# Kernel optimization log

Measured on AMD Instinct MI355X. Metric: run time of the kernel, lower is better.

## Reference

```python
import jax, jax.numpy as jnp
import numpy as np

HEADS = 8
DIM_HEAD = 64
WINDOW = 8  # local_window_size


def _sn_weight(W, u, sigma):
    """SNLinear reparameterized weight: one power-iteration step (detached)
    then sigma_W = v^T W u (grad flows through W only), weight = W/sigma_W * sigma."""
    v = W @ u
    v = v / jnp.linalg.norm(v)
    u2 = W.T @ v
    u2 = u2 / jnp.linalg.norm(u2)
    v = jax.lax.stop_gradient(v)
    u2 = jax.lax.stop_gradient(u2)
    sigma_w = jnp.einsum('c,cd,d->', v, W, u2)
    return W / sigma_w * sigma


def setup_inputs() -> dict:
    key = jax.random.key(0)
    ks = jax.random.split(key, 6)
    B, S, D = 2, 2048, 512
    inner = HEADS * DIM_HEAD  # 512
    x = jax.random.normal(ks[0], (B, S, D), dtype=jnp.float32)
    W_qkv = 0.02 * jax.random.normal(ks[1], (3 * inner, D), dtype=jnp.float32)
    u_qkv = jax.random.normal(ks[2], (D,), dtype=jnp.float32)
    u_qkv = u_qkv / jnp.linalg.norm(u_qkv)
    W_out = 0.02 * jax.random.normal(ks[3], (D, inner), dtype=jnp.float32)
    b_out = jnp.zeros((D,), dtype=jnp.float32)
    u_out = jax.random.normal(ks[4], (inner,), dtype=jnp.float32)
    u_out = u_out / jnp.linalg.norm(u_out)
    sigma_qkv = jnp.ones((1,), dtype=jnp.float32)
    sigma_out = jnp.ones((1,), dtype=jnp.float32)
    temperature = jnp.asarray(np.log(DIM_HEAD ** -0.5), dtype=jnp.float32)
    return {
        'x': x, 'W_qkv': W_qkv, 'u_qkv': u_qkv, 'sigma_qkv': sigma_qkv,
        'W_out': W_out, 'b_out': b_out, 'u_out': u_out, 'sigma_out': sigma_out,
        'temperature': temperature,
    }


def reference(x, W_qkv, u_qkv, sigma_qkv, W_out, b_out, u_out, sigma_out, temperature):
    B, S, D = x.shape
    # qkv projection (spectral-normed, no bias)
    Wq = _sn_weight(W_qkv, u_qkv, sigma_qkv[0])
    qkv = x @ Wq.T                                   # [B,S,3*inner]
    q, k, v = jnp.split(qkv, 3, axis=-1)
    to_heads = lambda t: t.reshape(B, S, HEADS, DIM_HEAD).transpose(0, 2, 1, 3)
    q, k, v = to_heads(q), to_heads(k), to_heads(v)   # [B,H,S,Dh]
    dots = jnp.einsum('bhid,bhjd->bhij', q, k) * jnp.exp(temperature)
    # local causal band mask (True inside band); original masked_fill fills True
    i = jnp.arange(S)
    band = (i[:, None] >= i[None, :]) & ((i[:, None] - i[None, :]) <= (WINDOW - 1))
    neg = -jnp.finfo(dots.dtype).max
    dots = jnp.where(band[None, None, :, :], neg, dots)
    attn = jax.nn.softmax(dots, axis=-1)
    out = jnp.einsum('bhij,bhjd->bhid', attn, v)      # [B,H,S,Dh]
    out = out.transpose(0, 2, 1, 3).reshape(B, S, HEADS * DIM_HEAD)
    Wo = _sn_weight(W_out, u_out, sigma_out[0])
    return out @ Wo.T + b_out
```

## Files before the change

kernel.cpp:

```cpp
#include <hip/hip_runtime.h>
#include <hip/hip_bf16.h>
#include <math.h>

#define HEADS 8
#define DH 64
#define SEQ 2048
#define BATCH 2
#define DMODEL 512
#define INNER 512
#define WIN 8

typedef unsigned short ushort_t;
typedef __attribute__((ext_vector_type(8))) __bf16 bf16x8;
typedef __attribute__((ext_vector_type(8))) unsigned short u16x8;
typedef __attribute__((ext_vector_type(4))) float f32x4;

__device__ inline float bf2f(ushort_t u) {
    unsigned v = ((unsigned)u) << 16; float f; __builtin_memcpy(&f, &v, 4); return f;
}
__device__ inline ushort_t f2bf(float f) {
    __hip_bfloat16 h = __float2bfloat16(f); ushort_t u; __builtin_memcpy(&u, &h, 2); return u;
}
__device__ inline float fast_exp2(float x) { return __builtin_amdgcn_exp2f(x); }
__device__ inline int swz_idx(int row, int col) { return ((row << 6) | col) ^ ((row & 7) << 3); }

__device__ inline bf16x8 ld_frag(const ushort_t* lds, int row, int col) {
    u16x8 v = *(const u16x8*)&lds[swz_idx(row, col)];
    return __builtin_bit_cast(bf16x8, v);
}
__device__ inline f32x4 mfma16(bf16x8 a, bf16x8 b, f32x4 c) {
    return __builtin_amdgcn_mfma_f32_16x16x32_bf16(a, b, c, 0, 0, 0);
}
__device__ inline void gload16(const void* g, void* l) {
    __builtin_amdgcn_global_load_lds(
        (const __attribute__((address_space(1))) unsigned int*)g,
        (__attribute__((address_space(3))) unsigned int*)l, 16, 0, 0);
}

__global__ __launch_bounds__(256) void fused_cast_sn1(const float* __restrict__ x,
                                                      const float* __restrict__ Wq,
                                                      const float* __restrict__ Wo,
                                                      const float* __restrict__ uq,
                                                      const float* __restrict__ uo,
                                                      ushort_t* __restrict__ xb,
                                                      ushort_t* __restrict__ wqb,
                                                      ushort_t* __restrict__ wob,
                                                      float* __restrict__ zbuf,
                                                      float* __restrict__ v1,
                                                      float* __restrict__ v2) {
    const int b = blockIdx.x;
    if (b < 1536) {
        const int gid = b * 256 + threadIdx.x;
        const float* src; ushort_t* dst; int g;
        if (gid < 262144)      { src = x;  dst = xb;  g = gid; }
        else if (gid < 360448) { src = Wq; dst = wqb; g = gid - 262144; }
        else                   { src = Wo; dst = wob; g = gid - 360448; }
        float4 a = *(const float4*)&src[(size_t)g * 8];
        float4 c = *(const float4*)&src[(size_t)g * 8 + 4];
        u16x8 o;
        o[0] = f2bf(a.x); o[1] = f2bf(a.y); o[2] = f2bf(a.z); o[3] = f2bf(a.w);
        o[4] = f2bf(c.x); o[5] = f2bf(c.y); o[6] = f2bf(c.z); o[7] = f2bf(c.w);
        *(u16x8*)&dst[(size_t)g * 8] = o;
        if (gid < 1032) zbuf[gid] = 0.f;
    } else {
        const int lane = threadIdx.x & 63, w = threadIdx.x >> 6;
        const int r = (b - 1536) * 4 + w;
        const float* W; const float* u; float* vout; int rr;
        if (r < 1536) { W = Wq; u = uq; vout = v1; rr = r; }
        else          { W = Wo; u = uo; vout = v2; rr = r - 1536; }
        float4 w0 = *(const float4*)&W[(size_t)rr * 512 + lane * 8];
        float4 w1 = *(const float4*)&W[(size_t)rr * 512 + lane * 8 + 4];
        float4 u0 = *(const float4*)&u[lane * 8];
        float4 u1 = *(const float4*)&u[lane * 8 + 4];
        float dot = w0.x * u0.x + w0.y * u0.y + w0.z * u0.z + w0.w * u0.w +
                    w1.x * u1.x + w1.y * u1.y + w1.z * u1.z + w1.w * u1.w;
#pragma unroll
        for (int off = 1; off < 64; off <<= 1) dot += __shfl_xor(dot, off, 64);
        if (lane == 0) vout[rr] = dot;
    }
}

__global__ __launch_bounds__(256) void gemm_qkv_sn(const ushort_t* __restrict__ A,
                                                   const ushort_t* __restrict__ B,
                                                   ushort_t* __restrict__ qkv,
                                                   const float* __restrict__ Wq,
                                                   const float* __restrict__ Wo,
                                                   const float* __restrict__ v1,
                                                   const float* __restrict__ v2,
                                                   float* __restrict__ z1,
                                                   float* __restrict__ z2,
                                                   float* __restrict__ counter,
                                                   const float* __restrict__ sq,
                                                   const float* __restrict__ so,
                                                   float* __restrict__ scales) {
    constexpr int K = DMODEL;
    __shared__ ushort_t As[8 * 128 * 8];
    __shared__ ushort_t Bs[8 * 64 * 8];
    __shared__ float red[256];
    __shared__ int is_last;
    const int t = threadIdx.x;

    if (blockIdx.x >= 768) {
        const int b = blockIdx.x - 768;
        {
            const float* W; const float* v; float* z; int r0;
            if (b < 96) { W = Wq; v = v1; z = z1; r0 = b * 16; }
            else        { W = Wo; v = v2; z = z2; r0 = (b - 96) * 16; }
            float a0 = 0.f, a1 = 0.f;
            for (int i = 0; i < 16; ++i) {
                float vv = v[r0 + i];
                a0 += W[(size_t)(r0 + i) * 512 + t] * vv;
                a1 += W[(size_t)(r0 + i) * 512 + 256 + t] * vv;
            }
            atomicAdd(&z[t], a0);
            atomicAdd(&z[t + 256], a1);
        }
        __threadfence();
        __syncthreads();
        if (t == 0) is_last = (atomicAdd(counter, 1.0f) == 127.0f);
        __syncthreads();
        if (!is_last) return;
        __threadfence();
        for (int which = 0; which < 2; ++which) {
            const float* v = which ? v2 : v1;
            const float* z = which ? z2 : z1;
            const int R = which ? 512 : 1536;
            float n1 = 0.f;
            for (int i = t; i < R; i += 256) { float q = v[i]; n1 += q * q; }
            red[t] = n1; __syncthreads();
            for (int off = 128; off > 0; off >>= 1) { if (t < off) red[t] += red[t + off]; __syncthreads(); }
            n1 = red[0]; __syncthreads();
            float n2 = 0.f;
            for (int i = t; i < 512; i += 256) { float q = z[i]; n2 += q * q; }
            red[t] = n2; __syncthreads();
            for (int off = 128; off > 0; off >>= 1) { if (t < off) red[t] += red[t + off]; __syncthreads(); }
            if (t == 0) scales[which] = (which ? so[0] : sq[0]) * sqrtf(n1 / red[0]);
            __syncthreads();
        }
        return;
    }

    const int lane = t & 63, w = t >> 6;
    const int wm = w >> 1, wn = w & 1, lg = lane >> 4, li = lane & 15;
    const int m0 = (blockIdx.x / 24) * 128, n0 = (blockIdx.x % 24) * 64;
    f32x4 acc[4][2] = {};
    for (int k0 = 0; k0 < K; k0 += 64) {
        __syncthreads();
#pragma unroll
        for (int i = 0; i < 4; ++i) {
            int j = w * 4 + i;
            int kc = j >> 1, mh = (j & 1) * 64;
            gload16(&A[(size_t)(m0 + mh + lane) * K + k0 + kc * 8], &As[(kc * 128 + mh) * 8]);
        }
#pragma unroll
        for (int i = 0; i < 2; ++i) {
            int kc = w * 2 + i;
            gload16(&B[(size_t)(n0 + lane) * K + k0 + kc * 8], &Bs[(kc * 64) * 8]);
        }
        __syncthreads();
#pragma unroll
        for (int kw = 0; kw < 2; ++kw) {
            bf16x8 af[4], bf[2];
#pragma unroll
            for (int mi = 0; mi < 4; ++mi)
                af[mi] = *(const bf16x8*)&As[((kw * 4 + lg) * 128 + wm * 64 + mi * 16 + li) * 8];
#pragma unroll
            for (int ni = 0; ni < 2; ++ni)
                bf[ni] = *(const bf16x8*)&Bs[((kw * 4 + lg) * 64 + wn * 32 + ni * 16 + li) * 8];
#pragma unroll
            for (int mi = 0; mi < 4; ++mi)
#pragma unroll
                for (int ni = 0; ni < 2; ++ni)
                    acc[mi][ni] = mfma16(af[mi], bf[ni], acc[mi][ni]);
        }
    }
    ushort_t* vT = qkv + (size_t)2 * BATCH * HEADS * SEQ * DH;
    if (n0 >= 1024) {
#pragma unroll
        for (int mi = 0; mi < 4; ++mi) {
            int base = m0 + wm * 64 + mi * 16 + lg * 4;
            int bb = base >> 11, ss = base & 2047;
#pragma unroll
            for (int ni = 0; ni < 2; ++ni) {
                int n = n0 + wn * 32 + ni * 16 + li;
                int h = (n >> 6) & 7, d0 = n & 63;
                ushort4 o;
                o.x = f2bf(acc[mi][ni][0]); o.y = f2bf(acc[mi][ni][1]);
                o.z = f2bf(acc[mi][ni][2]); o.w = f2bf(acc[mi][ni][3]);
                *(ushort4*)&vT[((size_t)((bb * HEADS + h) * DH) + d0) * SEQ + ss] = o;
            }
        }
    } else {
#pragma unroll
        for (int mi = 0; mi < 4; ++mi)
#pragma unroll
            for (int r = 0; r < 4; ++r) {
                int row = m0 + wm * 64 + mi * 16 + lg * 4 + r;
                int bb = row >> 11, ss = row & 2047;
#pragma unroll
                for (int ni = 0; ni < 2; ++ni) {
                    int n = n0 + wn * 32 + ni * 16 + li;
                    int which = n >> 9, h = (n >> 6) & 7, d0 = n & 63;
                    qkv[(size_t)which * (BATCH * HEADS * SEQ * DH) +
                        ((size_t)((bb * HEADS + h) * SEQ) + ss) * DH + d0] = f2bf(acc[mi][ni][r]);
                }
            }
    }
}

__global__ __launch_bounds__(256) void gemm_bt_out(const ushort_t* __restrict__ A,
                                                   const ushort_t* __restrict__ B,
                                                   const float* __restrict__ scales,
                                                   const float* __restrict__ bias,
                                                   float* __restrict__ C) {
    constexpr int K = INNER;
    __shared__ ushort_t As[8 * 64 * 8];
    __shared__ ushort_t Bs[8 * 64 * 8];
    const int t = threadIdx.x, lane = t & 63, w = t >> 6;
    const int wm = w >> 1, wn = w & 1, lg = lane >> 4, li = lane & 15;
    const int m0 = blockIdx.y * 64, n0 = blockIdx.x * 64;
    f32x4 acc[2][2] = {};
    for (int k0 = 0; k0 < K; k0 += 64) {
        __syncthreads();
#pragma unroll
        for (int i = 0; i < 2; ++i) {
            int kc = w * 2 + i;
            gload16(&A[(size_t)(m0 + lane) * K + k0 + kc * 8], &As[(kc * 64) * 8]);
            gload16(&B[(size_t)(n0 + lane) * K + k0 + kc * 8], &Bs[(kc * 64) * 8]);
        }
        __syncthreads();
#pragma unroll
        for (int kw = 0; kw < 2; ++kw) {
            bf16x8 af[2], bf[2];
#pragma unroll
            for (int mi = 0; mi < 2; ++mi)
                af[mi] = *(const bf16x8*)&As[((kw * 4 + lg) * 64 + wm * 32 + mi * 16 + li) * 8];
#pragma unroll
            for (int ni = 0; ni < 2; ++ni)
                bf[ni] = *(const bf16x8*)&Bs[((kw * 4 + lg) * 64 + wn * 32 + ni * 16 + li) * 8];
#pragma unroll
            for (int mi = 0; mi < 2; ++mi)
#pragma unroll
                for (int ni = 0; ni < 2; ++ni)
                    acc[mi][ni] = mfma16(af[mi], bf[ni], acc[mi][ni]);
        }
    }
    const float sc = scales[0] * scales[1];
#pragma unroll
    for (int mi = 0; mi < 2; ++mi)
#pragma unroll
        for (int r = 0; r < 4; ++r) {
            int row = m0 + wm * 32 + mi * 16 + lg * 4 + r;
#pragma unroll
            for (int ni = 0; ni < 2; ++ni) {
                int n = n0 + wn * 32 + ni * 16 + li;
                C[(size_t)row * INNER + n] = acc[mi][ni][r] * sc + bias[n];
            }
        }
}

__global__ __launch_bounds__(512) void attn_mfma_kernel(const ushort_t* __restrict__ qkv,
                                                        const float* __restrict__ temp,
                                                        const float* __restrict__ scales,
                                                        ushort_t* __restrict__ attn_out) {
    __shared__ ushort_t kvbuf[2 * 4 * 4096];
    __shared__ ushort_t Pl[2 * 4096];
    const int t    = threadIdx.x;
    const int lane = t & 63, w = t >> 6;
    const int g    = w >> 2, wl = w & 3;
    const int lg   = lane >> 4, li = lane & 15;
    const int bh   = blockIdx.x >> 5;
    const int i0   = (blockIdx.x & 31) * 64;
    const ushort_t* qp  = qkv;
    const ushort_t* kp  = qkv + (size_t)BATCH * HEADS * SEQ * DH;
    const ushort_t* vTp = kp  + (size_t)BATCH * HEADS * SEQ * DH;
    const ushort_t* kp_bh  = kp  + (size_t)bh * SEQ * DH;
    const ushort_t* vTp_bh = vTp + (size_t)bh * DH * SEQ;
    const float s0 = scales[0];
    const float st = expf(temp[0]) * s0 * s0 * 1.44269504088896340736f;

    ushort_t* Pb = Pl + g * 4096;
    const int srw = lane >> 3;
    const int sc  = (lane & 7) ^ srw;

    bf16x8 aQ[2];
#pragma unroll
    for (int c = 0; c < 2; ++c) {
        u16x8 qv = *(const u16x8*)&qp[((size_t)bh * SEQ + i0 + 16 * wl + li) * DH + 32 * c + lg * 8];
        u16x8 r;
#pragma unroll
        for (int j = 0; j < 8; ++j) r[j] = f2bf(bf2f(qv[j]) * st);
        aQ[c] = __builtin_bit_cast(bf16x8, r);
    }

    float lsum = 0.f;
    f32x4 oacc[4] = {};
    const int qi = i0 + 16 * wl + li;

    auto STAGE = [&](int jtn, int tbuf) {
#pragma unroll
        for (int i = 0; i < 4; ++i) {
            const int sid = i * 8 + w;
            const int bsel = sid >> 3;
            const int srow8 = sid & 7;
            const int row = srow8 * 8 + srw;
            const ushort_t* gsrc;
            if (bsel < 2)
                gsrc = kp_bh + (size_t)(jtn * 128 + bsel * 64 + row) * DH + sc * 8;
            else
                gsrc = vTp_bh + (size_t)row * SEQ + jtn * 128 + (bsel - 2) * 64 + sc * 8;
            gload16(gsrc, &kvbuf[tbuf * 16384 + bsel * 4096 + srow8 * 512]);
        }
    };

    STAGE(0, 0);
    __syncthreads();

    int cur = 0;
    for (int jt = 0; jt < SEQ / 128; ++jt) {
        if (jt < SEQ / 128 - 1) STAGE(jt + 1, cur ^ 1);
        const ushort_t* Kb = kvbuf + cur * 16384 + g * 4096;
        const ushort_t* Vb = kvbuf + cur * 16384 + 8192 + g * 4096;
        const int j0 = jt * 128 + g * 64;

        f32x4 s[4];
        __builtin_amdgcn_s_setprio(1);
#pragma unroll
        for (int kc = 0; kc < 4; ++kc) {
            bf16x8 b0 = ld_frag(Kb, kc * 16 + li, lg * 8);
            bf16x8 b1 = ld_frag(Kb, kc * 16 + li, 32 + lg * 8);
            f32x4 z = {0.f, 0.f, 0.f, 0.f};
            z = mfma16(b0, aQ[0], z);
            z = mfma16(b1, aQ[1], z);
            s[kc] = z;
        }
        __builtin_amdgcn_s_setprio(0);
        const bool need_mask = (j0 == i0) || (j0 == i0 - 64);
#pragma unroll
        for (int kc = 0; kc < 4; ++kc) {
            float p0, p1, p2, p3;
            if (need_mask) {
                int kjb = j0 + kc * 16 + lg * 4;
                p0 = ((unsigned)(qi - kjb - 0) < (unsigned)WIN) ? 0.f : fast_exp2(s[kc][0]);
                p1 = ((unsigned)(qi - kjb - 1) < (unsigned)WIN) ? 0.f : fast_exp2(s[kc][1]);
                p2 = ((unsigned)(qi - kjb - 2) < (unsigned)WIN) ? 0.f : fast_exp2(s[kc][2]);
                p3 = ((unsigned)(qi - kjb - 3) < (unsigned)WIN) ? 0.f : fast_exp2(s[kc][3]);
            } else {
                p0 = fast_exp2(s[kc][0]); p1 = fast_exp2(s[kc][1]);
                p2 = fast_exp2(s[kc][2]); p3 = fast_exp2(s[kc][3]);
            }
            lsum += (p0 + p1) + (p2 + p3);
            ushort4 o;
            o.x = f2bf(p0); o.y = f2bf(p1); o.z = f2bf(p2); o.w = f2bf(p3);
            *(ushort4*)&Pb[swz_idx(16 * wl + li, kc * 16 + lg * 4)] = o;
        }
        bf16x8 aP[2];
#pragma unroll
        for (int c = 0; c < 2; ++c) aP[c] = ld_frag(Pb, 16 * wl + li, c * 32 + lg * 8);
        __builtin_amdgcn_s_setprio(1);
#pragma unroll
        for (int tt = 0; tt < 4; ++tt) {
            bf16x8 b0 = ld_frag(Vb, tt * 16 + li, lg * 8);
            bf16x8 b1 = ld_frag(Vb, tt * 16 + li, 32 + lg * 8);
            oacc[tt] = mfma16(aP[0], b0, oacc[tt]);
            oacc[tt] = mfma16(aP[1], b1, oacc[tt]);
        }
        __builtin_amdgcn_s_setprio(0);
        __syncthreads();
        cur ^= 1;
    }

    lsum += __shfl_xor(lsum, 16, 64);
    lsum += __shfl_xor(lsum, 32, 64);
    float* den    = (float*)Pl;
    float* O_part = (float*)kvbuf;
    if (lg == 0) den[g * 64 + 16 * wl + li] = lsum;
    if (g == 1) {
#pragma unroll
        for (int r = 0; r < 4; ++r) {
            int row = 16 * wl + lg * 4 + r;
#pragma unroll
            for (int tt = 0; tt < 4; ++tt)
                O_part[row * 68 + tt * 16 + li] = oacc[tt][r];
        }
    }
    __syncthreads();
    if (g == 0) {
        const int b_ = bh >> 3, h = bh & 7;
#pragma unroll
        for (int r = 0; r < 4; ++r) {
            int row = 16 * wl + lg * 4 + r;
            float inv = 1.0f / (den[row] + den[64 + row]);
            size_t base = ((size_t)(b_ * SEQ + i0 + row)) * INNER + h * DH;
#pragma unroll
            for (int tt = 0; tt < 4; ++tt)
                attn_out[base + tt * 16 + li] =
                    f2bf((oacc[tt][r] + O_part[row * 68 + tt * 16 + li]) * inv);
        }
    }
}

extern "C" void kernel_launch(void* const* d_in, const int* in_sizes, int n_in,
                              void* d_out, int out_size, void* d_ws, size_t ws_size,
                              hipStream_t stream) {
    const float* x     = (const float*)d_in[0];
    const float* W_qkv = (const float*)d_in[1];
    const float* u_qkv = (const float*)d_in[2];
    const float* s_qkv = (const float*)d_in[3];
    const float* W_out = (const float*)d_in[4];
    const float* b_out = (const float*)d_in[5];
    const float* u_out = (const float*)d_in[6];
    const float* s_out = (const float*)d_in[7];
    const float* temp  = (const float*)d_in[8];
    float* out = (float*)d_out;

    float* scales  = (float*)d_ws;
    float* v1      = scales + 64;
    float* v2      = v1 + 1536;
    float* z1      = v2 + 512;
    float* z2      = z1 + 512;
    float* counter = z1 + 1024;
    ushort_t* xb    = (ushort_t*)((char*)d_ws + 16384);
    ushort_t* wqb   = xb + (size_t)2097152;
    ushort_t* wob   = wqb + (size_t)786432;
    ushort_t* qkvb  = wob + (size_t)262144;
    ushort_t* attnb = qkvb + (size_t)6291456;

    fused_cast_sn1<<<dim3(2048), dim3(256), 0, stream>>>(x, W_qkv, W_out, u_qkv, u_out,
                                                         xb, wqb, wob, z1, v1, v2);
    gemm_qkv_sn<<<dim3(896), dim3(256), 0, stream>>>(xb, wqb, qkvb, W_qkv, W_out, v1, v2,
                                                     z1, z2, counter, s_qkv, s_out, scales);
    attn_mfma_kernel<<<dim3(512), dim3(512), 0, stream>>>(qkvb, temp, scales, attnb);
    gemm_bt_out<<<dim3(8, 64), dim3(256), 0, stream>>>(attnb, wob, scales, b_out, out);
}
```

Baseline: 164.1 us.

## Double-buffer LDS tiles in QKV and output GEMMs; schedule power-iteration blocks first

```diff
diff --git a/kernel.cpp b/kernel.cpp
--- a/kernel.cpp
+++ b/kernel.cpp
@@ -94,14 +94,14 @@
                                                    const float* __restrict__ so,
                                                    float* __restrict__ scales) {
     constexpr int K = DMODEL;
-    __shared__ ushort_t As[8 * 128 * 8];
-    __shared__ ushort_t Bs[8 * 64 * 8];
+    __shared__ ushort_t As[2][8 * 128 * 8];
+    __shared__ ushort_t Bs[2][8 * 64 * 8];
     __shared__ float red[256];
     __shared__ int is_last;
     const int t = threadIdx.x;
 
-    if (blockIdx.x >= 768) {
-        const int b = blockIdx.x - 768;
+    if (blockIdx.x < 128) {
+        const int b = blockIdx.x;
         {
             const float* W; const float* v; float* z; int r0;
             if (b < 96) { W = Wq; v = v1; z = z1; r0 = b * 16; }
@@ -140,39 +140,49 @@
         return;
     }
 
+    const int bid = blockIdx.x - 128;
     const int lane = t & 63, w = t >> 6;
     const int wm = w >> 1, wn = w & 1, lg = lane >> 4, li = lane & 15;
-    const int m0 = (blockIdx.x / 24) * 128, n0 = (blockIdx.x % 24) * 64;
+    const int m0 = (bid / 24) * 128, n0 = (bid % 24) * 64;
     f32x4 acc[4][2] = {};
-    for (int k0 = 0; k0 < K; k0 += 64) {
-        __syncthreads();
+
+    auto STAGE = [&](int ks, int buf) {
+        const int k0 = ks * 64;
 #pragma unroll
         for (int i = 0; i < 4; ++i) {
             int j = w * 4 + i;
             int kc = j >> 1, mh = (j & 1) * 64;
-            gload16(&A[(size_t)(m0 + mh + lane) * K + k0 + kc * 8], &As[(kc * 128 + mh) * 8]);
+            gload16(&A[(size_t)(m0 + mh + lane) * K + k0 + kc * 8], &As[buf][(kc * 128 + mh) * 8]);
         }
 #pragma unroll
         for (int i = 0; i < 2; ++i) {
             int kc = w * 2 + i;
-            gload16(&B[(size_t)(n0 + lane) * K + k0 + kc * 8], &Bs[(kc * 64) * 8]);
-        }
-        __syncthreads();
+            gload16(&B[(size_t)(n0 + lane) * K + k0 + kc * 8], &Bs[buf][(kc * 64) * 8]);
+        }
+    };
+
+    STAGE(0, 0);
+    __syncthreads();
+    int cur = 0;
+    for (int ks = 0; ks < K / 64; ++ks) {
+        if (ks < K / 64 - 1) STAGE(ks + 1, cur ^ 1);
 #pragma unroll
         for (int kw = 0; kw < 2; ++kw) {
             bf16x8 af[4], bf[2];
 #pragma unroll
             for (int mi = 0; mi < 4; ++mi)
-                af[mi] = *(const bf16x8*)&As[((kw * 4 + lg) * 128 + wm * 64 + mi * 16 + li) * 8];
+                af[mi] = *(const bf16x8*)&As[cur][((kw * 4 + lg) * 128 + wm * 64 + mi * 16 + li) * 8];
 #pragma unroll
             for (int ni = 0; ni < 2; ++ni)
-                bf[ni] = *(const bf16x8*)&Bs[((kw * 4 + lg) * 64 + wn * 32 + ni * 16 + li) * 8];
+                bf[ni] = *(const bf16x8*)&Bs[cur][((kw * 4 + lg) * 64 + wn * 32 + ni * 16 + li) * 8];
 #pragma unroll
             for (int mi = 0; mi < 4; ++mi)
 #pragma unroll
                 for (int ni = 0; ni < 2; ++ni)
                     acc[mi][ni] = mfma16(af[mi], bf[ni], acc[mi][ni]);
         }
+        __syncthreads();
+        cur ^= 1;
     }
     ushort_t* vT = qkv + (size_t)2 * BATCH * HEADS * SEQ * DH;
     if (n0 >= 1024) {
@@ -214,36 +224,45 @@
                                                    const float* __restrict__ bias,
                                                    float* __restrict__ C) {
     constexpr int K = INNER;
-    __shared__ ushort_t As[8 * 64 * 8];
-    __shared__ ushort_t Bs[8 * 64 * 8];
+    __shared__ ushort_t As[2][8 * 64 * 8];
+    __shared__ ushort_t Bs[2][8 * 64 * 8];
     const int t = threadIdx.x, lane = t & 63, w = t >> 6;
     const int wm = w >> 1, wn = w & 1, lg = lane >> 4, li = lane & 15;
     const int m0 = blockIdx.y * 64, n0 = blockIdx.x * 64;
     f32x4 acc[2][2] = {};
-    for (int k0 = 0; k0 < K; k0 += 64) {
-        __syncthreads();
+
+    auto STAGE = [&](int ks, int buf) {
+        const int k0 = ks * 64;
 #pragma unroll
         for (int i = 0; i < 2; ++i) {
             int kc = w * 2 + i;
-            gload16(&A[(size_t)(m0 + lane) * K + k0 + kc * 8], &As[(kc * 64) * 8]);
-            gload16(&B[(size_t)(n0 + lane) * K + k0 + kc * 8], &Bs[(kc * 64) * 8]);
-        }
-        __syncthreads();
+            gload16(&A[(size_t)(m0 + lane) * K + k0 + kc * 8], &As[buf][(kc * 64) * 8]);
+            gload16(&B[(size_t)(n0 + lane) * K + k0 + kc * 8], &Bs[buf][(kc * 64) * 8]);
+        }
+    };
+
+    STAGE(0, 0);
+    __syncthreads();
+    int cur = 0;
+    for (int ks = 0; ks < K / 64; ++ks) {
+        if (ks < K / 64 - 1) STAGE(ks + 1, cur ^ 1);
 #pragma unroll
         for (int kw = 0; kw < 2; ++kw) {
             bf16x8 af[2], bf[2];
 #pragma unroll
             for (int mi = 0; mi < 2; ++mi)
-                af[mi] = *(const bf16x8*)&As[((kw * 4 + lg) * 64 + wm * 32 + mi * 16 + li) * 8];
+                af[mi] = *(const bf16x8*)&As[cur][((kw * 4 + lg) * 64 + wm * 32 + mi * 16 + li) * 8];
 #pragma unroll
             for (int ni = 0; ni < 2; ++ni)
-                bf[ni] = *(const bf16x8*)&Bs[((kw * 4 + lg) * 64 + wn * 32 + ni * 16 + li) * 8];
+                bf[ni] = *(const bf16x8*)&Bs[cur][((kw * 4 + lg) * 64 + wn * 32 + ni * 16 + li) * 8];
 #pragma unroll
             for (int mi = 0; mi < 2; ++mi)
 #pragma unroll
                 for (int ni = 0; ni < 2; ++ni)
                     acc[mi][ni] = mfma16(af[mi], bf[ni], acc[mi][ni]);
         }
+        __syncthreads();
+        cur ^= 1;
     }
     const float sc = scales[0] * scales[1];
 #pragma unroll
```

Measured after the change: 158.9 us. 1.03x faster.
